# Kernel optimization log

Measured on AMD Instinct MI355X. Metric: run time of the kernel, lower is better.

The kernel has to match this reference:

```python
import jax, jax.numpy as jnp
import numpy as np

N = 100000   # nodes
E = 1600000  # edges (avg degree 16)
D = 128      # input feature dim
H = 64       # hidden dim (hard-coded in Sage.__init__)
C = 40       # output classes


def setup_inputs() -> dict:
    key = jax.random.key(0)
    ks = jax.random.split(key, 9)
    s_in = 1.0 / np.sqrt(D)
    s_h = 1.0 / np.sqrt(H)
    return {
        "x": jax.random.normal(ks[0], (N, D), jnp.float32),
        "edge_index": jax.random.randint(ks[1], (2, E), 0, N, dtype=jnp.int64),
        # SAGEConv params: lin_l acts on aggregated neighbors (carries bias),
        # lin_r acts on the root/self features (no bias), per PyG defaults.
        "W1_l": jax.random.uniform(ks[2], (D, H), jnp.float32, -s_in, s_in),
        "W1_r": jax.random.uniform(ks[3], (D, H), jnp.float32, -s_in, s_in),
        "b1": jax.random.uniform(ks[4], (H,), jnp.float32, -s_in, s_in),
        "W2_l": jax.random.uniform(ks[5], (H, C), jnp.float32, -s_h, s_h),
        "W2_r": jax.random.uniform(ks[6], (H, C), jnp.float32, -s_h, s_h),
        "b2": jax.random.uniform(ks[7], (C,), jnp.float32, -s_h, s_h),
    }


def _sage_conv(x, src, dst, W_l, W_r, b):
    # mean-aggregate neighbor features at destination nodes
    msg = x[src]                                             # [E, F] gather
    summed = jax.ops.segment_sum(msg, dst, num_segments=N)   # [N, F]
    deg = jax.ops.segment_sum(jnp.ones((src.shape[0],), x.dtype), dst,
                              num_segments=N)                # [N]
    agg = summed / jnp.maximum(deg, 1.0)[:, None]
    return agg @ W_l + x @ W_r + b


def reference(x, edge_index, W1_l, W1_r, b1, W2_l, W2_r, b2):
    src, dst = edge_index[0], edge_index[1]
    h = _sage_conv(x, src, dst, W1_l, W1_r, b1)
    h = jax.nn.relu(h)
    # F.dropout(training=False) in eval mode -> identity
    out = _sage_conv(h, src, dst, W2_l, W2_r, b2)
    return jax.nn.log_softmax(out, axis=1)
```

## Files before the change

kernel.cpp:

```cpp
#include <hip/hip_runtime.h>

__device__ __forceinline__ float bf2f(unsigned short u) {
  union { unsigned int i; float f; } c; c.i = ((unsigned int)u) << 16; return c.f;
}
__device__ __forceinline__ unsigned short f2bf(float f) {
  union { float f; unsigned int i; } c; c.f = f;
  unsigned int x = c.i;
  return (unsigned short)((x + 0x7fffu + ((x >> 16) & 1u)) >> 16);
}
__device__ __forceinline__ float lo16(unsigned int w) { return bf2f((unsigned short)(w & 0xffffu)); }
__device__ __forceinline__ float hi16(unsigned int w) { return bf2f((unsigned short)(w >> 16)); }

#define DD 128
#define HH 64
#define CC 40
#define NBUCK 512
#define NCHUNK 256
#define MAXNPB 256
#define NQ 4
#define NR 4
#define ECAP 6144

using bf16x8 = __attribute__((ext_vector_type(8))) short;
using f32x4  = __attribute__((ext_vector_type(4))) float;

__global__ __launch_bounds__(256) void detect_prepw_hist(
    const unsigned int* e32u, const unsigned int* x32, int* flags,
    const void* W1l, const void* W1r, const void* b1,
    const void* W2l, const void* W2r, const void* b2,
    unsigned short* Wb1, unsigned short* Wb2, float* b1f, float* b2f,
    const int* e32, int E, int N, unsigned mulM, int* histG) {
  __shared__ int cnt[NBUCK * NR];
  int tid = threadIdx.x;
  int b = blockIdx.x;

  if (b == 0) {
    unsigned int v = 0;
    for (int i = tid; i < 4096; i += 256) v |= e32u[2 * i + 1];
    int c2 = 0;
    for (int i = tid; i < 4096; i += 256) {
      unsigned int w = x32[i];
      unsigned int expo = (w >> 7) & 0xffu;
      unsigned short lo = (unsigned short)(w & 0xffffu);
      if (lo == 0 || (expo >= 100u && expo <= 133u)) c2++;
    }
    cnt[tid] = (int)v; cnt[256 + tid] = c2; __syncthreads();
    for (int s = 128; s > 0; s >>= 1) {
      if (tid < s) { cnt[tid] |= cnt[tid + s]; cnt[256 + tid] += cnt[256 + tid + s]; }
      __syncthreads();
    }
    if (tid == 0) {
      flags[0] = (cnt[0] == 0) ? 1 : 0;
      flags[1] = (cnt[256] < 2048) ? 1 : 0;
    }
    return;
  }

  if (b <= 2) {
    const unsigned int* w32 = (const unsigned int*)W1l;
    int c2 = 0;
    for (int i = tid; i < 4096; i += 256) {
      unsigned int w = w32[i];
      unsigned int expo = (w >> 7) & 0xffu;
      unsigned short lo = (unsigned short)(w & 0xffffu);
      if (lo == 0 || (expo >= 100u && expo <= 133u)) c2++;
    }
    cnt[tid] = c2; __syncthreads();
    for (int s = 128; s > 0; s >>= 1) {
      if (tid < s) cnt[tid] += cnt[tid + s];
      __syncthreads();
    }
    int isf = (cnt[0] < 2048) ? 1 : 0;
    auto rd = [&](const void* p, int i) -> float {
      return isf ? ((const float*)p)[i] : bf2f(((const unsigned short*)p)[i]);
    };
    if (b == 1) {
      for (int idx = tid; idx < 128 * 128; idx += 256) {
        int n = idx >> 7, k = idx & 127;
        float v = (n < HH) ? rd(W1l, k * HH + n) : rd(W1r, k * HH + (n - HH));
        Wb1[idx] = f2bf(v);
      }
    } else {
      for (int idx = tid; idx < 48 * 128; idx += 256) {
        int n = idx >> 7, k = idx & 127;
        float v = 0.f;
        if (n < CC) v = (k < HH) ? rd(W2l, k * CC + n) : rd(W2r, (k - HH) * CC + n);
        Wb2[idx] = f2bf(v);
      }
      if (tid < HH) b1f[tid] = rd(b1, tid);
      if (tid < CC) b2f[tid] = rd(b2, tid);
    }
    return;
  }

  int hb = b - 3;
  unsigned int v = 0;
  for (int i = tid; i < 4096; i += 256) v |= e32u[2 * i + 1];
  cnt[tid] = (int)v; __syncthreads();
  for (int s = 128; s > 0; s >>= 1) {
    if (tid < s) cnt[tid] |= cnt[tid + s];
    __syncthreads();
  }
  int isI64 = (cnt[0] == 0) ? 1 : 0;
  __syncthreads();
  for (int i = tid; i < NBUCK * NR; i += 256) cnt[i] = 0;
  __syncthreads();
  int rep = tid & (NR - 1);
  int chunk = (E + NCHUNK - 1) / NCHUNK;
  int e0 = hb * chunk, e1 = min(e0 + chunk, E);
  for (int i = e0 + tid; i < e1; i += 256) {
    int d = isI64 ? e32[2 * (E + i)] : e32[E + i];
    d = min(max(d, 0), N - 1);
    int bk = (int)__umulhi((unsigned)d, mulM);
    atomicAdd(&cnt[bk * NR + rep], 1);
  }
  __syncthreads();
  for (int i = tid; i < NBUCK; i += 256)
    histG[i * NCHUNK + hb] =
        cnt[i * NR] + cnt[i * NR + 1] + cnt[i * NR + 2] + cnt[i * NR + 3];
}

__global__ __launch_bounds__(256) void scanA(const int* histG, int* ohist, int* bsum) {
  __shared__ int t[NCHUNK];
  int b = blockIdx.x, tid = threadIdx.x;
  int v = histG[b * NCHUNK + tid];
  t[tid] = v; __syncthreads();
  for (int st = 1; st < NCHUNK; st <<= 1) {
    int u = (tid >= st) ? t[tid - st] : 0;
    __syncthreads();
    t[tid] += u;
    __syncthreads();
  }
  ohist[b * NCHUNK + tid] = t[tid] - v;
  if (tid == NCHUNK - 1) bsum[b] = t[tid];
}

__global__ __launch_bounds__(512) void scanB(const int* bsum, int* bbase,
                                             int* row_ptr4, int N, int E) {
  __shared__ int t[NBUCK];
  int tid = threadIdx.x;
  int v = bsum[tid];
  t[tid] = v; __syncthreads();
  for (int st = 1; st < NBUCK; st <<= 1) {
    int u = (tid >= st) ? t[tid - st] : 0;
    __syncthreads();
    t[tid] += u;
    __syncthreads();
  }
  bbase[tid] = t[tid] - v;
  if (tid == 0) { bbase[NBUCK] = E; row_ptr4[NQ * N] = E; }
}

__global__ __launch_bounds__(256) void scat_or_t1(
    const int* e32, int E, int N, const int* flags, int nodesPerB,
    unsigned mulM, int qshift, const int* ohist, const int* bbase, unsigned* ebuf,
    const void* xraw, const unsigned short* Wb1, const float* b1f,
    unsigned short* t1, unsigned short* s1, int T1B) {
  __shared__ int cur[NBUCK];
  int b = blockIdx.x;
  int tid = threadIdx.x;

  if (b < NCHUNK) {
    for (int i = tid; i < NBUCK; i += 256)
      cur[i] = ohist[i * NCHUNK + b] + bbase[i];
    __syncthreads();
    int isI64 = flags[0];
    int chunk = (E + NCHUNK - 1) / NCHUNK;
    int e0 = b * chunk, e1 = min(e0 + chunk, E);
    for (int i = e0 + tid; i < e1; i += 256) {
      int s, d;
      if (isI64) { s = e32[2 * i]; d = e32[2 * (E + i)]; }
      else       { s = e32[i];     d = e32[E + i]; }
      s = min(max(s, 0), N - 1);
      d = min(max(d, 0), N - 1);
      int bk = (int)__umulhi((unsigned)d, mulM);
      int ld = d - bk * nodesPerB;
      unsigned q = (unsigned)s >> qshift;
      int p = atomicAdd(&cur[bk], 1);
      ebuf[p] = ((unsigned)ld << 19) | (q << 17) | (unsigned)s;
    }
    return;
  }

  int t = b - NCHUNK;
  if (t >= T1B) return;
  int lane = tid & 63, wv = tid >> 6;
  int nb = t * 64 + wv * 16;
  int oc = lane & 15, kgrp = lane >> 4;
  int node = min(nb + oc, N - 1);
  f32x4 acc[8];
#pragma unroll
  for (int i = 0; i < 8; i++) acc[i] = (f32x4){0.f, 0.f, 0.f, 0.f};

  if (flags[1]) {
    const float4* x4 = (const float4*)xraw;
#pragma unroll
    for (int kb = 0; kb < 4; kb++) {
      int k0 = kb * 32 + kgrp * 8;
      float4 a0 = x4[(size_t)node * 32 + (k0 >> 2)];
      float4 a1 = x4[(size_t)node * 32 + (k0 >> 2) + 1];
      bf16x8 af;
      af[0] = (short)f2bf(a0.x); af[1] = (short)f2bf(a0.y);
      af[2] = (short)f2bf(a0.z); af[3] = (short)f2bf(a0.w);
      af[4] = (short)f2bf(a1.x); af[5] = (short)f2bf(a1.y);
      af[6] = (short)f2bf(a1.z); af[7] = (short)f2bf(a1.w);
#pragma unroll
      for (int nblk = 0; nblk < 8; nblk++) {
        bf16x8 bfr = *(const bf16x8*)&Wb1[(nblk * 16 + oc) * 128 + k0];
        acc[nblk] = __builtin_amdgcn_mfma_f32_16x16x32_bf16(af, bfr, acc[nblk], 0, 0, 0);
      }
    }
  } else {
    const unsigned short* x16 = (const unsigned short*)xraw;
#pragma unroll
    for (int kb = 0; kb < 4; kb++) {
      int k0 = kb * 32 + kgrp * 8;
      bf16x8 af = *(const bf16x8*)&x16[(size_t)node * 128 + k0];
#pragma unroll
      for (int nblk = 0; nblk < 8; nblk++) {
        bf16x8 bfr = *(const bf16x8*)&Wb1[(nblk * 16 + oc) * 128 + k0];
        acc[nblk] = __builtin_amdgcn_mfma_f32_16x16x32_bf16(af, bfr, acc[nblk], 0, 0, 0);
      }
    }
  }

  int r0 = kgrp * 4;
#pragma unroll
  for (int nblk = 0; nblk < 8; nblk++) {
    float bias = (nblk >= 4) ? b1f[(nblk - 4) * 16 + oc] : 0.f;
#pragma unroll
    for (int r = 0; r < 4; r++) {
      int nn = nb + r0 + r;
      if (nn < N) {
        if (nblk < 4)
          t1[(size_t)nn * HH + nblk * 16 + oc] = f2bf(acc[nblk][r]);
        else
          s1[(size_t)nn * HH + (nblk - 4) * 16 + oc] = f2bf(acc[nblk][r] + bias);
      }
    }
  }
}

__global__ __launch_bounds__(256) void bktB(
    const unsigned* ebuf, const int* bbase,
    int nodesPerB, int* row_ptr4, float* invd, int* col, int N) {
  __shared__ unsigned ecache[ECAP];
  __shared__ int cnt[MAXNPB * NQ];
  __shared__ int sA[256];
  int b = blockIdx.x;
  int tid = threadIdx.x;
  int base_node = b * nodesPerB;
  int nn = min(nodesPerB, N - base_node);
  if (nn <= 0) return;
  int nk = nn * NQ;
  int eb0 = bbase[b], eb1 = bbase[b + 1];
  int nE = eb1 - eb0;
  const unsigned* ee = ebuf + eb0;
  bool useL = (nE <= ECAP);
  for (int i = tid; i < nk; i += 256) cnt[i] = 0;
  __syncthreads();
  if (useL) {
    for (int i = tid; i < nE; i += 256) {
      unsigned v = ee[i];
      ecache[i] = v;
      atomicAdd(&cnt[v >> 17], 1);
    }
  } else {
    for (int i = tid; i < nE; i += 256) atomicAdd(&cnt[ee[i] >> 17], 1);
  }
  __syncthreads();
  for (int i = tid; i < nn; i += 256) {
    int d = cnt[NQ * i] + cnt[NQ * i + 1] + cnt[NQ * i + 2] + cnt[NQ * i + 3];
    invd[base_node + i] = 1.0f / (float)max(d, 1);
  }
  __syncthreads();
  int per = (nk + 255) / 256;
  int myb = tid * per;
  int dreg[4];
  int ssum = 0;
#pragma unroll
  for (int k = 0; k < 4; k++) {
    int idx = myb + k;
    int v = (k < per && idx < nk) ? cnt[idx] : 0;
    dreg[k] = v; ssum += v;
  }
  sA[tid] = ssum;
  __syncthreads();
  for (int st = 1; st < 256; st <<= 1) {
    int t = (tid >= st) ? sA[tid - st] : 0;
    __syncthreads();
    sA[tid] += t;
    __syncthreads();
  }
  int run = eb0 + sA[tid] - ssum;
  __syncthreads();
#pragma unroll
  for (int k = 0; k < 4; k++) {
    int idx = myb + k;
    if (k < per && idx < nk) {
      row_ptr4[(size_t)(base_node + (idx >> 2)) * NQ + (idx & 3)] = run;
      cnt[idx] = run;
      run += dreg[k];
    }
  }
  __syncthreads();
  if (useL) {
    for (int i = tid; i < nE; i += 256) {
      unsigned v = ecache[i];
      int p = atomicAdd(&cnt[v >> 17], 1);
      col[p] = (int)(v & 0x1FFFFu);
    }
  } else {
    for (int i = tid; i < nE; i += 256) {
      unsigned v = ee[i];
      int p = atomicAdd(&cnt[v >> 17], 1);
      col[p] = (int)(v & 0x1FFFFu);
    }
  }
}

__device__ __forceinline__ void gather_seg(const uint4* t8, const int* col,
                                           int s0, int s1, int r, int c,
                                           float acc[8]) {
  for (int base = s0; base < s1; base += 4) {
    int i = base + r;
    bool g = (i < s1);
    int nb = g ? col[i] : 0;
    uint4 v = make_uint4(0, 0, 0, 0);
    if (g) v = t8[(size_t)nb * 8 + c];
    acc[0] += lo16(v.x); acc[1] += hi16(v.x);
    acc[2] += lo16(v.y); acc[3] += hi16(v.y);
    acc[4] += lo16(v.z); acc[5] += hi16(v.z);
    acc[6] += lo16(v.w); acc[7] += hi16(v.w);
  }
}

__global__ __launch_bounds__(256) void aggregate1(const unsigned short* t1,
                                                  const unsigned short* s1,
                                                  const int* row_ptr4, const float* invd,
                                                  const int* col, unsigned short* h, int N) {
  int wave = threadIdx.x >> 6, lane = threadIdx.x & 63;
  int ns = lane >> 5, r = (lane >> 3) & 3, c = lane & 7;
  int n = blockIdx.x * 8 + wave * 2 + ns;
  if (n >= N) return;
  int4 rp = *(const int4*)&row_ptr4[(size_t)NQ * n];
  int e4 = row_ptr4[(size_t)NQ * n + 4];
  float acc[8] = {0, 0, 0, 0, 0, 0, 0, 0};
  const uint4* t8 = (const uint4*)t1;
  gather_seg(t8, col, rp.x, rp.y, r, c, acc);
  gather_seg(t8, col, rp.y, rp.z, r, c, acc);
  gather_seg(t8, col, rp.z, rp.w, r, c, acc);
  gather_seg(t8, col, rp.w, e4, r, c, acc);
#pragma unroll
  for (int m = 8; m <= 16; m <<= 1)
#pragma unroll
    for (int i = 0; i < 8; i++) acc[i] += __shfl_xor(acc[i], m, 64);

  if (r == 0) {
    float id = invd[n];
    uint4 sv = ((const uint4*)s1)[(size_t)n * 8 + c];
    float s[8] = {lo16(sv.x), hi16(sv.x), lo16(sv.y), hi16(sv.y),
                  lo16(sv.z), hi16(sv.z), lo16(sv.w), hi16(sv.w)};
    unsigned int o[4];
#pragma unroll
    for (int i = 0; i < 4; i++) {
      float a0 = fmaxf(acc[2 * i] * id + s[2 * i], 0.f);
      float a1 = fmaxf(acc[2 * i + 1] * id + s[2 * i + 1], 0.f);
      o[i] = (unsigned int)f2bf(a0) | ((unsigned int)f2bf(a1) << 16);
    }
    ((uint4*)h)[(size_t)n * 8 + c] = make_uint4(o[0], o[1], o[2], o[3]);
  }
}

__global__ __launch_bounds__(256) void agg2f(const unsigned short* h,
                                             const int* row_ptr4, const float* invd,
                                             const int* col,
                                             const unsigned short* Wb2,
                                             const float* b2f,
                                             float* out, int N) {
  __shared__ unsigned lds[64 * 33];
  int tid = threadIdx.x, wv = tid >> 6, lane = tid & 63;
  int ns = lane >> 5, r = (lane >> 3) & 3, c = lane & 7;
  int nb = blockIdx.x * 64;
  const uint4* h8 = (const uint4*)h;

  for (int rr = 0; rr < 8; rr++) {
    int ln = wv * 16 + rr * 2 + ns;
    int n = nb + ln;
    float acc[8] = {0, 0, 0, 0, 0, 0, 0, 0};
    int4 rp; int e4;
    if (n < N) {
      rp = *(const int4*)&row_ptr4[(size_t)NQ * n];
      e4 = row_ptr4[(size_t)NQ * n + 4];
    } else {
      rp = make_int4(0, 0, 0, 0); e4 = 0;
    }
    gather_seg(h8, col, rp.x, rp.y, r, c, acc);
    gather_seg(h8, col, rp.y, rp.z, r, c, acc);
    gather_seg(h8, col, rp.z, rp.w, r, c, acc);
    gather_seg(h8, col, rp.w, e4, r, c, acc);
#pragma unroll
    for (int m = 8; m <= 16; m <<= 1)
#pragma unroll
      for (int i = 0; i < 8; i++) acc[i] += __shfl_xor(acc[i], m, 64);
    if (r == 0) {
      float id = (n < N) ? invd[n] : 0.f;
#pragma unroll
      for (int q = 0; q < 4; q++) {
        unsigned u = (unsigned)f2bf(acc[2 * q] * id) |
                     ((unsigned)f2bf(acc[2 * q + 1] * id) << 16);
        lds[ln * 33 + c * 4 + q] = u;
      }
    }
  }
  __syncthreads();

  int oc = lane & 15, kgrp = lane >> 4;
  int noderow = wv * 16 + oc;
  int node = min(nb + noderow, N - 1);
  f32x4 acc3[3];
#pragma unroll
  for (int i = 0; i < 3; i++) acc3[i] = (f32x4){0.f, 0.f, 0.f, 0.f};

#pragma unroll
  for (int kb = 0; kb < 4; kb++) {
    int k0 = kb * 32 + kgrp * 8;
    bf16x8 af;
    if (kb < 2) {
      union { unsigned u[4]; bf16x8 v; } cv;
      int base = noderow * 33 + (k0 >> 1);
      cv.u[0] = lds[base]; cv.u[1] = lds[base + 1];
      cv.u[2] = lds[base + 2]; cv.u[3] = lds[base + 3];
      af = cv.v;
    } else {
      af = *(const bf16x8*)&h[(size_t)node * HH + (k0 - 64)];
    }
#pragma unroll
    for (int nblk = 0; nblk < 3; nblk++) {
      bf16x8 bfr = *(const bf16x8*)&Wb2[(nblk * 16 + oc) * 128 + k0];
      acc3[nblk] = __builtin_amdgcn_mfma_f32_16x16x32_bf16(af, bfr, acc3[nblk], 0, 0, 0);
    }
  }

#pragma unroll
  for (int nblk = 0; nblk < 3; nblk++) {
    int cc = nblk * 16 + oc;
    float bias = (cc < CC) ? b2f[cc] : 0.f;
#pragma unroll
    for (int rg = 0; rg < 4; rg++) acc3[nblk][rg] += bias;
  }

#pragma unroll
  for (int rg = 0; rg < 4; rg++) {
    int nn = nb + wv * 16 + kgrp * 4 + rg;
    float m = -INFINITY;
#pragma unroll
    for (int nblk = 0; nblk < 3; nblk++)
      if (nblk * 16 + oc < CC) m = fmaxf(m, acc3[nblk][rg]);
    for (int off = 1; off <= 8; off <<= 1) m = fmaxf(m, __shfl_xor(m, off, 64));
    float s = 0.f;
#pragma unroll
    for (int nblk = 0; nblk < 3; nblk++)
      if (nblk * 16 + oc < CC) s += __expf(acc3[nblk][rg] - m);
    for (int off = 1; off <= 8; off <<= 1) s += __shfl_xor(s, off, 64);
    float lse = m + __logf(s);
    if (nn < N) {
#pragma unroll
      for (int nblk = 0; nblk < 3; nblk++) {
        int cc = nblk * 16 + oc;
        if (cc < CC) out[(size_t)nn * CC + cc] = acc3[nblk][rg] - lse;
      }
    }
  }
}

extern "C" void kernel_launch(void* const* d_in, const int* in_sizes, int n_in,
                              void* d_out, int out_size, void* d_ws, size_t ws_size,
                              hipStream_t stream) {
  const void* x   = d_in[0];
  const int*  e   = (const int*)d_in[1];
  const void* W1l = d_in[2];
  const void* W1r = d_in[3];
  const void* b1  = d_in[4];
  const void* W2l = d_in[5];
  const void* W2r = d_in[6];
  const void* b2  = d_in[7];
  float* out = (float*)d_out;

  const int N = in_sizes[0] / DD;
  const int E = in_sizes[1] / 2;
  const int nodesPerB = (N + NBUCK - 1) / NBUCK;
  const int nbuck = (N + nodesPerB - 1) / nodesPerB;
  const unsigned mulM =
      (unsigned)(((1ULL << 32) + (unsigned)nodesPerB - 1) / (unsigned)nodesPerB);
  const int T1B = (N + 63) / 64;
  int qshift = 0;
  while (((unsigned)(N - 1) >> qshift) > 3u) qshift++;

  char* w = (char*)d_ws;
  size_t off = 0;
  auto carve = [&](size_t bytes) -> void* {
    void* p = (void*)(w + off);
    off += (bytes + 255) & ~(size_t)255;
    return p;
  };
  int* col      = (int*)carve((size_t)E * 4);
  int* row_ptr4 = (int*)carve(((size_t)N * NQ + 1) * 4);
  float* invd   = (float*)carve((size_t)N * 4);
  int* histG    = (int*)carve((size_t)NBUCK * NCHUNK * 4);
  int* ohist    = (int*)carve((size_t)NBUCK * NCHUNK * 4);
  int* bsum     = (int*)carve(NBUCK * 4);
  int* bbase    = (int*)carve((NBUCK + 1) * 4);
  int* flags    = (int*)carve(8);
  unsigned short* t1   = (unsigned short*)carve((size_t)N * HH * 2);
  unsigned short* s1   = (unsigned short*)carve((size_t)N * HH * 2);
  unsigned short* h    = (unsigned short*)carve((size_t)N * HH * 2);
  unsigned short* Wb1  = (unsigned short*)carve(128 * 128 * 2);
  unsigned short* Wb2  = (unsigned short*)carve(48 * 128 * 2);
  float* b1f   = (float*)carve(HH * sizeof(float));
  float* b2f   = (float*)carve(CC * sizeof(float));
  unsigned* ebuf = (unsigned*)carve((size_t)E * 4);
  (void)ws_size; (void)n_in; (void)out_size;

  detect_prepw_hist<<<3 + NCHUNK, 256, 0, stream>>>(
      (const unsigned int*)e, (const unsigned int*)x, flags,
      W1l, W1r, b1, W2l, W2r, b2, Wb1, Wb2, b1f, b2f,
      e, E, N, mulM, histG);
  scanA<<<NBUCK, NCHUNK, 0, stream>>>(histG, ohist, bsum);
  scanB<<<1, 512, 0, stream>>>(bsum, bbase, row_ptr4, N, E);
  scat_or_t1<<<NCHUNK + T1B, 256, 0, stream>>>(e, E, N, flags, nodesPerB,
                                               mulM, qshift, ohist, bbase, ebuf,
                                               x, Wb1, b1f, t1, s1, T1B);
  bktB<<<nbuck, 256, 0, stream>>>(ebuf, bbase, nodesPerB, row_ptr4, invd, col, N);
  aggregate1<<<(N + 7) / 8, 256, 0, stream>>>(t1, s1, row_ptr4, invd, col, h, N);
  agg2f<<<(N + 63) / 64, 256, 0, stream>>>(h, row_ptr4, invd, col, Wb2, b2f, out, N);
}
```

Before: 293.6 us.

## Drop source-quadrant sub-bucketing of CSR; use plain row_ptr and halve scatter blocks

Removes the four-way split of each destination's neighbor list by source-index quadrant, so the CSR becomes a plain row_ptr with one segment per node. The bucket kernel's count, scan and fill shrink to one counter per node, and the aggregation kernels make one gather_seg call instead of four. Separately, the scatter phase now uses 128 blocks that each cover two histogram chunks. This loses whatever gather locality the quadrant ordering gave and leaves fewer blocks to run the scatter in parallel.

```diff
diff --git a/kernel.cpp b/kernel.cpp
--- a/kernel.cpp
+++ b/kernel.cpp
@@ -16,8 +16,8 @@
 #define CC 40
 #define NBUCK 512
 #define NCHUNK 256
+#define NSCAT 128
 #define MAXNPB 256
-#define NQ 4
 #define NR 4
 #define ECAP 6144
 
@@ -136,7 +136,7 @@
 }
 
 __global__ __launch_bounds__(512) void scanB(const int* bsum, int* bbase,
-                                             int* row_ptr4, int N, int E) {
+                                             int* row_ptr, int N, int E) {
   __shared__ int t[NBUCK];
   int tid = threadIdx.x;
   int v = bsum[tid];
@@ -148,25 +148,25 @@
     __syncthreads();
   }
   bbase[tid] = t[tid] - v;
-  if (tid == 0) { bbase[NBUCK] = E; row_ptr4[NQ * N] = E; }
+  if (tid == 0) { bbase[NBUCK] = E; row_ptr[N] = E; }
 }
 
 __global__ __launch_bounds__(256) void scat_or_t1(
     const int* e32, int E, int N, const int* flags, int nodesPerB,
-    unsigned mulM, int qshift, const int* ohist, const int* bbase, unsigned* ebuf,
+    unsigned mulM, const int* ohist, const int* bbase, unsigned* ebuf,
     const void* xraw, const unsigned short* Wb1, const float* b1f,
     unsigned short* t1, unsigned short* s1, int T1B) {
   __shared__ int cur[NBUCK];
   int b = blockIdx.x;
   int tid = threadIdx.x;
 
-  if (b < NCHUNK) {
+  if (b < NSCAT) {
     for (int i = tid; i < NBUCK; i += 256)
-      cur[i] = ohist[i * NCHUNK + b] + bbase[i];
+      cur[i] = ohist[i * NCHUNK + 2 * b] + bbase[i];
     __syncthreads();
     int isI64 = flags[0];
     int chunk = (E + NCHUNK - 1) / NCHUNK;
-    int e0 = b * chunk, e1 = min(e0 + chunk, E);
+    int e0 = 2 * b * chunk, e1 = min(e0 + 2 * chunk, E);
     for (int i = e0 + tid; i < e1; i += 256) {
       int s, d;
       if (isI64) { s = e32[2 * i]; d = e32[2 * (E + i)]; }
@@ -175,14 +175,13 @@
       d = min(max(d, 0), N - 1);
       int bk = (int)__umulhi((unsigned)d, mulM);
       int ld = d - bk * nodesPerB;
-      unsigned q = (unsigned)s >> qshift;
       int p = atomicAdd(&cur[bk], 1);
-      ebuf[p] = ((unsigned)ld << 19) | (q << 17) | (unsigned)s;
+      ebuf[p] = ((unsigned)ld << 17) | (unsigned)s;
     }
     return;
   }
 
-  int t = b - NCHUNK;
+  int t = b - NSCAT;
   if (t >= T1B) return;
   int lane = tid & 63, wv = tid >> 6;
   int nb = t * 64 + wv * 16;
@@ -243,21 +242,20 @@
 
 __global__ __launch_bounds__(256) void bktB(
     const unsigned* ebuf, const int* bbase,
-    int nodesPerB, int* row_ptr4, float* invd, int* col, int N) {
+    int nodesPerB, int* row_ptr, float* invd, int* col, int N) {
   __shared__ unsigned ecache[ECAP];
-  __shared__ int cnt[MAXNPB * NQ];
+  __shared__ int cnt[MAXNPB];
   __shared__ int sA[256];
   int b = blockIdx.x;
   int tid = threadIdx.x;
   int base_node = b * nodesPerB;
   int nn = min(nodesPerB, N - base_node);
   if (nn <= 0) return;
-  int nk = nn * NQ;
   int eb0 = bbase[b], eb1 = bbase[b + 1];
   int nE = eb1 - eb0;
   const unsigned* ee = ebuf + eb0;
   bool useL = (nE <= ECAP);
-  for (int i = tid; i < nk; i += 256) cnt[i] = 0;
+  for (int i = tid; i < nn; i += 256) cnt[i] = 0;
   __syncthreads();
   if (useL) {
     for (int i = tid; i < nE; i += 256) {
@@ -269,22 +267,9 @@
     for (int i = tid; i < nE; i += 256) atomicAdd(&cnt[ee[i] >> 17], 1);
   }
   __syncthreads();
-  for (int i = tid; i < nn; i += 256) {
-    int d = cnt[NQ * i] + cnt[NQ * i + 1] + cnt[NQ * i + 2] + cnt[NQ * i + 3];
-    invd[base_node + i] = 1.0f / (float)max(d, 1);
-  }
-  __syncthreads();
-  int per = (nk + 255) / 256;
-  int myb = tid * per;
-  int dreg[4];
-  int ssum = 0;
-#pragma unroll
-  for (int k = 0; k < 4; k++) {
-    int idx = myb + k;
-    int v = (k < per && idx < nk) ? cnt[idx] : 0;
-    dreg[k] = v; ssum += v;
-  }
-  sA[tid] = ssum;
+  int deg = (tid < nn) ? cnt[tid] : 0;
+  if (tid < nn) invd[base_node + tid] = 1.0f / (float)max(deg, 1);
+  sA[tid] = deg;
   __syncthreads();
   for (int st = 1; st < 256; st <<= 1) {
     int t = (tid >= st) ? sA[tid - st] : 0;
@@ -292,16 +277,11 @@
     sA[tid] += t;
     __syncthreads();
   }
-  int run = eb0 + sA[tid] - ssum;
-  __syncthreads();
-#pragma unroll
-  for (int k = 0; k < 4; k++) {
-    int idx = myb + k;
-    if (k < per && idx < nk) {
-      row_ptr4[(size_t)(base_node + (idx >> 2)) * NQ + (idx & 3)] = run;
-      cnt[idx] = run;
-      run += dreg[k];
-    }
+  int run = eb0 + sA[tid] - deg;
+  __syncthreads();
+  if (tid < nn) {
+    row_ptr[base_node + tid] = run;
+    cnt[tid] = run;
   }
   __syncthreads();
   if (useL) {
@@ -337,20 +317,15 @@
 
 __global__ __launch_bounds__(256) void aggregate1(const unsigned short* t1,
                                                   const unsigned short* s1,
-                                                  const int* row_ptr4, const float* invd,
+                                                  const int* row_ptr, const float* invd,
                                                   const int* col, unsigned short* h, int N) {
   int wave = threadIdx.x >> 6, lane = threadIdx.x & 63;
   int ns = lane >> 5, r = (lane >> 3) & 3, c = lane & 7;
   int n = blockIdx.x * 8 + wave * 2 + ns;
   if (n >= N) return;
-  int4 rp = *(const int4*)&row_ptr4[(size_t)NQ * n];
-  int e4 = row_ptr4[(size_t)NQ * n + 4];
+  int s0 = row_ptr[n], s1e = row_ptr[n + 1];
   float acc[8] = {0, 0, 0, 0, 0, 0, 0, 0};
-  const uint4* t8 = (const uint4*)t1;
-  gather_seg(t8, col, rp.x, rp.y, r, c, acc);
-  gather_seg(t8, col, rp.y, rp.z, r, c, acc);
-  gather_seg(t8, col, rp.z, rp.w, r, c, acc);
-  gather_seg(t8, col, rp.w, e4, r, c, acc);
+  gather_seg((const uint4*)t1, col, s0, s1e, r, c, acc);
 #pragma unroll
   for (int m = 8; m <= 16; m <<= 1)
 #pragma unroll
@@ -373,7 +348,7 @@
 }
 
 __global__ __launch_bounds__(256) void agg2f(const unsigned short* h,
-                                             const int* row_ptr4, const float* invd,
+                                             const int* row_ptr, const float* invd,
                                              const int* col,
                                              const unsigned short* Wb2,
                                              const float* b2f,
@@ -388,17 +363,9 @@
     int ln = wv * 16 + rr * 2 + ns;
     int n = nb + ln;
     float acc[8] = {0, 0, 0, 0, 0, 0, 0, 0};
-    int4 rp; int e4;
-    if (n < N) {
-      rp = *(const int4*)&row_ptr4[(size_t)NQ * n];
-      e4 = row_ptr4[(size_t)NQ * n + 4];
-    } else {
-      rp = make_int4(0, 0, 0, 0); e4 = 0;
-    }
-    gather_seg(h8, col, rp.x, rp.y, r, c, acc);
-    gather_seg(h8, col, rp.y, rp.z, r, c, acc);
-    gather_seg(h8, col, rp.z, rp.w, r, c, acc);
-    gather_seg(h8, col, rp.w, e4, r, c, acc);
+    int s0 = 0, s1e = 0;
+    if (n < N) { s0 = row_ptr[n]; s1e = row_ptr[n + 1]; }
+    gather_seg(h8, col, s0, s1e, r, c, acc);
 #pragma unroll
     for (int m = 8; m <= 16; m <<= 1)
 #pragma unroll
@@ -494,8 +461,6 @@
   const unsigned mulM =
       (unsigned)(((1ULL << 32) + (unsigned)nodesPerB - 1) / (unsigned)nodesPerB);
   const int T1B = (N + 63) / 64;
-  int qshift = 0;
-  while (((unsigned)(N - 1) >> qshift) > 3u) qshift++;
 
   char* w = (char*)d_ws;
   size_t off = 0;
@@ -505,7 +470,7 @@
     return p;
   };
   int* col      = (int*)carve((size_t)E * 4);
-  int* row_ptr4 = (int*)carve(((size_t)N * NQ + 1) * 4);
+  int* row_ptr  = (int*)carve(((size_t)N + 1) * 4);
   float* invd   = (float*)carve((size_t)N * 4);
   int* histG    = (int*)carve((size_t)NBUCK * NCHUNK * 4);
   int* ohist    = (int*)carve((size_t)NBUCK * NCHUNK * 4);
@@ -527,11 +492,11 @@
       W1l, W1r, b1, W2l, W2r, b2, Wb1, Wb2, b1f, b2f,
       e, E, N, mulM, histG);
   scanA<<<NBUCK, NCHUNK, 0, stream>>>(histG, ohist, bsum);
-  scanB<<<1, 512, 0, stream>>>(bsum, bbase, row_ptr4, N, E);
-  scat_or_t1<<<NCHUNK + T1B, 256, 0, stream>>>(e, E, N, flags, nodesPerB,
-                                               mulM, qshift, ohist, bbase, ebuf,
-                                               x, Wb1, b1f, t1, s1, T1B);
-  bktB<<<nbuck, 256, 0, stream>>>(ebuf, bbase, nodesPerB, row_ptr4, invd, col, N);
-  aggregate1<<<(N + 7) / 8, 256, 0, stream>>>(t1, s1, row_ptr4, invd, col, h, N);
-  agg2f<<<(N + 63) / 64, 256, 0, stream>>>(h, row_ptr4, invd, col, Wb2, b2f, out, N);
-}
+  scanB<<<1, 512, 0, stream>>>(bsum, bbase, row_ptr, N, E);
+  scat_or_t1<<<NSCAT + T1B, 256, 0, stream>>>(e, E, N, flags, nodesPerB,
+                                              mulM, ohist, bbase, ebuf,
+                                              x, Wb1, b1f, t1, s1, T1B);
+  bktB<<<nbuck, 256, 0, stream>>>(ebuf, bbase, nodesPerB, row_ptr, invd, col, N);
+  aggregate1<<<(N + 7) / 8, 256, 0, stream>>>(t1, s1, row_ptr, invd, col, h, N);
+  agg2f<<<(N + 63) / 64, 256, 0, stream>>>(h, row_ptr, invd, col, Wb2, b2f, out, N);
+}
```

Result: faster. 279.5 us (-4.8%).
